# Kernel tuning notes

Measured on AMD Instinct MI355X. Metric: run time of the kernel, lower is better.

The kernel has to match this reference:

```python
import jax, jax.numpy as jnp
import numpy as np

RPN_NEG_OV = 0.3
RPN_POS_OV = 0.7
RPN_BATCHSIZE = 256
NUM_FG = int(0.5 * RPN_BATCHSIZE)  # RPN_FG_FRACTION * RPN_BATCHSIZE


def _generate_anchors(base_size=16, ratios=(0.5, 1, 2), scales=(8, 16, 32)):
    base = np.array([1, 1, base_size, base_size], dtype=np.float64) - 1
    w = base[2] - base[0] + 1
    h = base[3] - base[1] + 1
    x_ctr = base[0] + 0.5 * (w - 1)
    y_ctr = base[1] + 0.5 * (h - 1)
    anchors = []
    for r in ratios:
        wr = w * np.sqrt(r)
        hr = h / np.sqrt(r)
        for s in scales:
            sw, sh = wr * s, hr * s
            anchors.append([x_ctr - 0.5 * (sw - 1), y_ctr - 0.5 * (sh - 1),
                            x_ctr + 0.5 * (sw - 1), y_ctr + 0.5 * (sh - 1)])
    return np.array(anchors, dtype=np.float32)  # (9,4)


def setup_inputs() -> dict:
    key = jax.random.key(0)
    k1, k2, k3, k4, k5 = jax.random.split(key, 5)
    H = W = 160
    A = 9
    im_h = im_w = 2560.0
    M = 128
    # valid GT boxes: centers in image, sizes 64..512
    cx = jax.random.uniform(k1, (M,), minval=200.0, maxval=im_w - 200.0)
    cy = jax.random.uniform(k2, (M,), minval=200.0, maxval=im_h - 200.0)
    wh = jax.random.uniform(k3, (M, 2), minval=64.0, maxval=512.0)
    x1 = jnp.clip(cx - 0.5 * wh[:, 0], 0.0, im_w - 2)
    y1 = jnp.clip(cy - 0.5 * wh[:, 1], 0.0, im_h - 2)
    x2 = jnp.clip(cx + 0.5 * wh[:, 0], x1 + 1.0, im_w - 1)
    y2 = jnp.clip(cy + 0.5 * wh[:, 1], y1 + 1.0, im_h - 1)
    gt_boxes = jnp.stack([x1, y1, x2, y2, jnp.ones((M,))], axis=1).astype(jnp.float32)
    return {
        "rpn_cls_score": jax.random.normal(k4, (1, 2 * A, H, W), dtype=jnp.float32),
        "gt_boxes": gt_boxes,
        "im_info": jnp.array([[im_h, im_w, 1.0]], dtype=jnp.float32),
        "anchors": jnp.asarray(_generate_anchors()),
        "rand_fg": jax.random.uniform(k5, (H * W * A,), dtype=jnp.float32),
        "rand_bg": jax.random.uniform(jax.random.fold_in(k5, 1), (H * W * A,), dtype=jnp.float32),
        "feat_stride": 16,
    }


def _forward(rpn_cls_score, gt_boxes, im_info, anchors, rand_fg, rand_bg, feat_stride):
    H, W = rpn_cls_score.shape[-2:]
    A = anchors.shape[0]
    # --- all anchors on the grid: (K*A, 4) ---
    sx = (jnp.arange(W, dtype=jnp.float32) * feat_stride)
    sy = (jnp.arange(H, dtype=jnp.float32) * feat_stride)
    gy, gx = jnp.meshgrid(sy, sx, indexing="ij")
    shifts = jnp.stack([gx.ravel(), gy.ravel(), gx.ravel(), gy.ravel()], axis=1)  # (K,4)
    all_anchors = (anchors[None, :, :] + shifts[:, None, :]).reshape(-1, 4)  # (T,4)
    T = all_anchors.shape[0]
    im = im_info[0]
    inside = ((all_anchors[:, 0] >= 0) & (all_anchors[:, 1] >= 0)
              & (all_anchors[:, 2] < im[1]) & (all_anchors[:, 3] < im[0]))  # (T,)

    # --- pairwise IoU (T, M), +1 pixel convention as in bbox_overlaps ---
    ax1, ay1, ax2, ay2 = (all_anchors[:, i] for i in range(4))
    gx1, gy1, gx2, gy2 = (gt_boxes[:, i] for i in range(4))
    a_area = (ax2 - ax1 + 1.0) * (ay2 - ay1 + 1.0)           # (T,)
    g_area = (gx2 - gx1 + 1.0) * (gy2 - gy1 + 1.0)           # (M,)
    iw = jnp.minimum(ax2[:, None], gx2[None, :]) - jnp.maximum(ax1[:, None], gx1[None, :]) + 1.0
    ih = jnp.minimum(ay2[:, None], gy2[None, :]) - jnp.maximum(ay1[:, None], gy1[None, :]) + 1.0
    inter = jnp.maximum(iw, 0.0) * jnp.maximum(ih, 0.0)      # (T,M)
    ov = inter / (a_area[:, None] + g_area[None, :] - inter)
    # outside anchors never participate (original gathers inside anchors first)
    ov = jnp.where(inside[:, None], ov, -1.0)

    argmax_ov = jnp.argmax(ov, axis=1)                        # (T,)
    max_ov = jnp.max(ov, axis=1)                              # (T,)
    gt_max = jnp.max(ov, axis=0)                              # (M,)
    is_best = jnp.any(ov == gt_max[None, :], axis=1)          # anchors achieving per-gt max

    # --- label assignment (RPN_CLOBBER_POSITIVES=False) ---
    labels = jnp.full((T,), -1.0, dtype=jnp.float32)
    labels = jnp.where(inside & (max_ov < RPN_NEG_OV), 0.0, labels)
    labels = jnp.where(is_best, 1.0, labels)
    labels = jnp.where(inside & (max_ov >= RPN_POS_OV), 1.0, labels)

    # --- subsample fg via random priorities (== randperm semantics) ---
    fg = labels == 1.0
    pr = jnp.where(fg, rand_fg, 2.0)                           # non-fg sort last
    rank = jnp.argsort(jnp.argsort(pr))
    labels = jnp.where(fg & (rank >= NUM_FG), -1.0, labels)

    # --- subsample bg ---
    num_bg = RPN_BATCHSIZE - jnp.sum(labels == 1.0)
    bg = labels == 0.0
    pr2 = jnp.where(bg, rand_bg, 2.0)
    rank2 = jnp.argsort(jnp.argsort(pr2))
    labels = jnp.where(bg & (rank2 >= num_bg), -1.0, labels)

    g = gt_boxes[argmax_ov, :4]                                # (T,4)
    ew = ax2 - ax1 + 1.0
    eh = ay2 - ay1 + 1.0
    ecx = ax1 + 0.5 * ew
    ecy = ay1 + 0.5 * eh
    gw = g[:, 2] - g[:, 0] + 1.0
    gh = g[:, 3] - g[:, 1] + 1.0
    gcx = g[:, 0] + 0.5 * gw
    gcy = g[:, 1] + 0.5 * gh
    targets = jnp.stack([(gcx - ecx) / ew, (gcy - ecy) / eh,
                         jnp.log(gw / ew), jnp.log(gh / eh)], axis=1)
    targets = jnp.where(inside[:, None], targets, 0.0)

    # --- weights ---
    inside_w = jnp.where((labels == 1.0)[:, None], 1.0, 0.0)   # RPN_BBOX_INSIDE_WEIGHTS = 1s
    num_examples = jnp.sum(labels >= 0.0).astype(jnp.float32)
    wgt = jnp.where(num_examples > 0, 1.0 / jnp.maximum(num_examples, 1.0), 0.0)
    outside_w = jnp.where((labels >= 0.0)[:, None], wgt, 0.0)

    # pack: [label | bbox_targets(4) | inside_w(4) | outside_w(4)] -> (T,13)
    return jnp.concatenate([labels[:, None], targets, inside_w, outside_w], axis=1)


def reference(rpn_cls_score, gt_boxes, im_info, anchors, rand_fg, rand_bg, feat_stride):
    return _forward(rpn_cls_score, gt_boxes, im_info, anchors, rand_fg, rand_bg, feat_stride)
```

## Files before the change

### kernel.cpp

```cpp
#include <hip/hip_runtime.h>
#include <cstdint>


#define T_TOTAL 230400
#define W_ 160
#define A_ 9
#define M_ 128
#define NB_ 900
#define NBINS 4096
#define BCAP 1024
#define KFG 128
#define BATCH 256
#define SSTR 17

struct Ws {
  int gt_max_bits[M_];
  float4 g_box[M_];
  float g_area[M_];
  float amm[4];
  int fg_count, bg_count;
  int bnd_fg_n, bnd_bg_n;
  int sel_fg, b_fg, cb_fg;
  int sel_bg, b_bg, cb_bg, k_bg;
  float cut_fg_val; int cut_fg_idx;
  float cut_bg_val; int cut_bg_idx;
  float wgt;
  int hist_fg[NBINS], hist_bg[NBINS];
  float bnd_fg_val[BCAP]; int bnd_fg_idx[BCAP];
  float bnd_bg_val[BCAP]; int bnd_bg_idx[BCAP];
  unsigned char lab8[T_TOTAL];
  float t_soa[4][T_TOTAL];
  int blk_max[NB_ * M_];
  float best_v[T_TOTAL];
  int best_j[T_TOTAL];
};

__device__ __forceinline__ float fA(float a, float b) { return __fadd_rn(a, b); }
__device__ __forceinline__ float fS(float a, float b) { return __fsub_rn(a, b); }
__device__ __forceinline__ float fM(float a, float b) { return __fmul_rn(a, b); }
__device__ __forceinline__ float fD(float a, float b) { return __fdiv_rn(a, b); }

__device__ __forceinline__ int bucket_of(float v) {
  int b = (int)(v * 4096.0f);
  return b > (NBINS - 1) ? (NBINS - 1) : (b < 0 ? 0 : b);
}

__device__ __forceinline__ void anchor_coords(int i, const float* anch, float fs,
                                              float& ax1, float& ay1, float& ax2, float& ay2) {
  int s = i / A_, a = i - s * A_;
  int x = s % W_, y = s / W_;
  float shx = fM((float)x, fs), shy = fM((float)y, fs);
  ax1 = fA(anch[a * 4 + 0], shx);
  ay1 = fA(anch[a * 4 + 1], shy);
  ax2 = fA(anch[a * 4 + 2], shx);
  ay2 = fA(anch[a * 4 + 3], shy);
}

__device__ __forceinline__ void wave_bbox(int i0, const float* amm, float fs,
                                          float imw, float imh,
                                          float& wx1, float& wy1, float& wx2, float& wy2) {
  int s_lo = i0 / A_, s_hi = (i0 + 63) / A_;
  int y_lo = s_lo / W_, y_hi = s_hi / W_;
  int x_lo = s_lo - y_lo * W_, x_hi = s_hi - y_hi * W_;
  if (y_lo != y_hi) { x_lo = 0; x_hi = W_ - 1; }
  wx1 = fmaxf(amm[0] + fM((float)x_lo, fs), 0.0f);
  wy1 = fmaxf(amm[1] + fM((float)y_lo, fs), 0.0f);
  wx2 = fminf(amm[2] + fM((float)x_hi, fs), imw);
  wy2 = fminf(amm[3] + fM((float)y_hi, fs), imh);
}

__global__ __launch_bounds__(256) void k_init(const float* gt, const float* anch, Ws* ws) {
  int t = blockIdx.x * blockDim.x + threadIdx.x;
  int n = gridDim.x * blockDim.x;
  for (int i = t; i < NBINS; i += n) { ws->hist_fg[i] = 0; ws->hist_bg[i] = 0; }
  if (t < M_) {
    float x1 = gt[t * 5 + 0], y1 = gt[t * 5 + 1];
    float x2 = gt[t * 5 + 2], y2 = gt[t * 5 + 3];
    ws->g_box[t] = make_float4(x1, y1, x2, y2);
    ws->g_area[t] = fM(fA(fS(x2, x1), 1.0f), fA(fS(y2, y1), 1.0f));
  }
  if (t == 0) {
    float mx1 = anch[0], my1 = anch[1], Mx2 = anch[2], My2 = anch[3];
    for (int a = 1; a < A_; ++a) {
      mx1 = fminf(mx1, anch[a * 4 + 0]);
      my1 = fminf(my1, anch[a * 4 + 1]);
      Mx2 = fmaxf(Mx2, anch[a * 4 + 2]);
      My2 = fmaxf(My2, anch[a * 4 + 3]);
    }
    ws->amm[0] = mx1; ws->amm[1] = my1; ws->amm[2] = Mx2; ws->amm[3] = My2;
    ws->fg_count = 0; ws->bg_count = 0;
    ws->bnd_fg_n = 0; ws->bnd_bg_n = 0;
    ws->cut_fg_val = 2.0f; ws->cut_fg_idx = 0x7fffffff;
    ws->cut_bg_val = 2.0f; ws->cut_bg_idx = 0x7fffffff;
  }
}

__global__ __launch_bounds__(256) void k_sweep(
    const float4* __restrict__ gbox, const float* __restrict__ gap,
    const float* __restrict__ amm,
    const float* im_info, const float* anchors, const int* fsp,
    int* __restrict__ blk_max, float* __restrict__ best_v, int* __restrict__ best_j) {
  __shared__ int smax[M_ * SSTR];
  int tid = threadIdx.x;
  for (int s = tid; s < M_ * SSTR; s += 256) smax[s] = 0;
  __syncthreads();

  int lane = tid & 63, wv = tid >> 6;
  int slot = lane & 15;
  int i = blockIdx.x * 256 + tid;
  float fs = (float)fsp[0];
  float imh = im_info[0], imw = im_info[1];
  float ax1, ay1, ax2, ay2;
  anchor_coords(i, anchors, fs, ax1, ay1, ax2, ay2);
  bool inside = (ax1 >= 0.0f) && (ay1 >= 0.0f) && (ax2 < imw) && (ay2 < imh);
  float aarea;
  if (inside) {
    aarea = fM(fA(fS(ax2, ax1), 1.0f), fA(fS(ay2, ay1), 1.0f));
  } else {
    ax1 = 0.0f; ay1 = 0.0f; ax2 = -2.0f; ay2 = -2.0f; aarea = 1.0f;
  }

  float wx1, wy1, wx2, wy2;
  wave_bbox(blockIdx.x * 256 + wv * 64, amm, fs, imw, imh, wx1, wy1, wx2, wy2);
  float4 gA = gbox[lane];
  float4 gB = gbox[lane + 64];
  bool cA = (gA.x <= wx2 + 1.0f) && (gA.z + 1.0f >= wx1) &&
            (gA.y <= wy2 + 1.0f) && (gA.w + 1.0f >= wy1);
  bool cB = (gB.x <= wx2 + 1.0f) && (gB.z + 1.0f >= wx1) &&
            (gB.y <= wy2 + 1.0f) && (gB.w + 1.0f >= wy1);
  unsigned long long m0 = __ballot(cA);
  unsigned long long m1 = __ballot(cB);

  float bestv = 0.0f;
  int bestj = 0;
  auto body = [&](int j) {
    float4 g = gbox[j];
    float iw = fA(fS(fminf(ax2, g.z), fmaxf(ax1, g.x)), 1.0f);
    float ih = fA(fS(fminf(ay2, g.w), fmaxf(ay1, g.y)), 1.0f);
    float inter = fM(fmaxf(iw, 0.0f), fmaxf(ih, 0.0f));
    float uni = fS(fA(aarea, gap[j]), inter);
    float ov = fD(inter, uni);
    if (ov > bestv) { bestv = ov; bestj = j; }
    if (ov > 0.0f) atomicMax(&smax[j * SSTR + slot], __float_as_int(ov));
  };
  while (m0) { int j = __ffsll(m0) - 1; m0 &= (m0 - 1); body(j); }
  while (m1) { int j = __ffsll(m1) + 63; m1 &= (m1 - 1); body(j); }

  best_v[i] = bestv;
  best_j[i] = bestj;
  __syncthreads();
  if (tid < M_) {
    int m = 0;
#pragma unroll
    for (int s = 0; s < 16; ++s) {
      int v = smax[tid * SSTR + s];
      m = v > m ? v : m;
    }
    blk_max[blockIdx.x * M_ + tid] = m;
  }
}

__global__ __launch_bounds__(64) void k_reduce(const int* __restrict__ blk_max, int* gmb) {
  int j = blockIdx.x;
  int lane = threadIdx.x;
  int m = 0;
  for (int b = lane; b < NB_; b += 64) {
    int v = blk_max[b * M_ + j];
    m = v > m ? v : m;
  }
  m = max(m, __shfl_xor(m, 1));
  m = max(m, __shfl_xor(m, 2));
  m = max(m, __shfl_xor(m, 4));
  m = max(m, __shfl_xor(m, 8));
  m = max(m, __shfl_xor(m, 16));
  m = max(m, __shfl_xor(m, 32));
  if (lane == 0) gmb[j] = m;
}

__global__ __launch_bounds__(256) void k_labels(
    const float4* __restrict__ gbox, const float* __restrict__ gap,
    const float* __restrict__ amm, const int* __restrict__ gmb,
    const int* __restrict__ blk_max,
    const float* __restrict__ best_v, const int* __restrict__ best_j,
    const float* im_info, const float* anchors, const int* fsp,
    const float* rand_fg, const float* rand_bg,
    Ws* ws) {
  int tid = threadIdx.x;
  int lane = tid & 63, wv = tid >> 6;
  int i = blockIdx.x * 256 + tid;
  float fs = (float)fsp[0];
  float imh = im_info[0], imw = im_info[1];
  float rx1, ry1, rx2, ry2;
  anchor_coords(i, anchors, fs, rx1, ry1, rx2, ry2);
  bool inside = (rx1 >= 0.0f) && (ry1 >= 0.0f) && (rx2 < imw) && (ry2 < imh);
  float ax1 = rx1, ay1 = ry1, ax2 = rx2, ay2 = ry2, aarea;
  if (inside) {
    aarea = fM(fA(fS(ax2, ax1), 1.0f), fA(fS(ay2, ay1), 1.0f));
  } else {
    ax1 = 0.0f; ay1 = 0.0f; ax2 = -2.0f; ay2 = -2.0f; aarea = 1.0f;
  }

  float wx1, wy1, wx2, wy2;
  wave_bbox(blockIdx.x * 256 + wv * 64, amm, fs, imw, imh, wx1, wy1, wx2, wy2);
  float4 gA = gbox[lane];
  float4 gB = gbox[lane + 64];
  bool cA = (gA.x <= wx2 + 1.0f) && (gA.z + 1.0f >= wx1) &&
            (gA.y <= wy2 + 1.0f) && (gA.w + 1.0f >= wy1);
  bool cB = (gB.x <= wx2 + 1.0f) && (gB.z + 1.0f >= wx1) &&
            (gB.y <= wy2 + 1.0f) && (gB.w + 1.0f >= wy1);
  unsigned long long m0 = __ballot(cA);
  unsigned long long m1 = __ballot(cB);

  float bestv = best_v[i];
  int bestj = best_j[i];
  bool isbest = false;
  const int* bmrow = blk_max + blockIdx.x * M_;
  auto body = [&](int j) {
    int gm = gmb[j];
    if (bmrow[j] != gm) return;
    float4 g = gbox[j];
    float iw = fA(fS(fminf(ax2, g.z), fmaxf(ax1, g.x)), 1.0f);
    float ih = fA(fS(fminf(ay2, g.w), fmaxf(ay1, g.y)), 1.0f);
    float inter = fM(fmaxf(iw, 0.0f), fmaxf(ih, 0.0f));
    float uni = fS(fA(aarea, gap[j]), inter);
    float ov = fD(inter, uni);
    if (__float_as_int(ov) == gm) isbest = true;
  };
  while (m0) { int j = __ffsll(m0) - 1; m0 &= (m0 - 1); body(j); }
  while (m1) { int j = __ffsll(m1) + 63; m1 &= (m1 - 1); body(j); }
  isbest = isbest && inside;

  float lab = -1.0f;
  if (inside && bestv < 0.3f) lab = 0.0f;
  if (isbest) lab = 1.0f;
  if (inside && bestv >= 0.7f) lab = 1.0f;

  float t0 = 0.0f, t1 = 0.0f, t2 = 0.0f, t3 = 0.0f;
  if (inside) {
    float ew = fA(fS(rx2, rx1), 1.0f), eh = fA(fS(ry2, ry1), 1.0f);
    float ecx = fA(rx1, fM(0.5f, ew)), ecy = fA(ry1, fM(0.5f, eh));
    float4 g = gbox[bestj];
    float gw = fA(fS(g.z, g.x), 1.0f), gh = fA(fS(g.w, g.y), 1.0f);
    float gcx = fA(g.x, fM(0.5f, gw)), gcy = fA(g.y, fM(0.5f, gh));
    t0 = fD(fS(gcx, ecx), ew);
    t1 = fD(fS(gcy, ecy), eh);
    t2 = logf(fD(gw, ew));
    t3 = logf(fD(gh, eh));
  }

  ws->lab8[i] = lab == 1.0f ? 2 : (lab == 0.0f ? 1 : 0);
  ws->t_soa[0][i] = t0;
  ws->t_soa[1][i] = t1;
  ws->t_soa[2][i] = t2;
  ws->t_soa[3][i] = t3;

  if (lab == 1.0f) atomicAdd(&ws->hist_fg[bucket_of(rand_fg[i])], 1);
  if (lab == 0.0f) atomicAdd(&ws->hist_bg[bucket_of(rand_bg[i])], 1);
}

__global__ __launch_bounds__(256) void k_scan(Ws* ws) {
  __shared__ int part[256];
  __shared__ int s_fgc;
  int tid = threadIdx.x;
  for (int pass = 0; pass < 2; ++pass) {
    const int* hist = pass == 0 ? ws->hist_fg : ws->hist_bg;
    int sum = 0;
    for (int b = 0; b < NBINS / 256; ++b) sum += hist[tid * (NBINS / 256) + b];
    part[tid] = sum;
    __syncthreads();
    if (tid == 0) {
      int cnt = 0;
      for (int c = 0; c < 256; ++c) cnt += part[c];
      int k, kbg = 0;
      if (pass == 0) {
        s_fgc = cnt;
        ws->fg_count = cnt;
        k = KFG;
      } else {
        ws->bg_count = cnt;
        int kept_fg = s_fgc < KFG ? s_fgc : KFG;
        kbg = BATCH - kept_fg;
        k = kbg;
      }
      if (cnt > k) {
        int cum = 0, chunk = 0;
        for (int c = 0; c < 256; ++c) {
          if (cum + part[c] >= k + 1) { chunk = c; break; }
          cum += part[c];
        }
        int b = chunk * (NBINS / 256);
        for (int bb = chunk * (NBINS / 256); bb < (chunk + 1) * (NBINS / 256); ++bb) {
          if (cum + hist[bb] >= k + 1) { b = bb; break; }
          cum += hist[bb];
        }
        if (pass == 0) { ws->sel_fg = 1; ws->b_fg = b; ws->cb_fg = cum; }
        else           { ws->sel_bg = 1; ws->b_bg = b; ws->cb_bg = cum; }
      } else {
        if (pass == 0) { ws->sel_fg = 0; ws->b_fg = -1; ws->cb_fg = 0; }
        else           { ws->sel_bg = 0; ws->b_bg = -1; ws->cb_bg = 0; }
      }
      if (pass == 1) ws->k_bg = kbg;
    }
    __syncthreads();
  }
}

__global__ __launch_bounds__(256) void k_collect(const float* rand_fg, const float* rand_bg,
                                                 Ws* ws) {
  int i = blockIdx.x * 256 + threadIdx.x;
  int code = ws->lab8[i];
  if (code == 2 && ws->sel_fg) {
    float v = rand_fg[i];
    if (bucket_of(v) == ws->b_fg) {
      int p = atomicAdd(&ws->bnd_fg_n, 1);
      if (p < BCAP) { ws->bnd_fg_val[p] = v; ws->bnd_fg_idx[p] = i; }
    }
  }
  if (code == 1 && ws->sel_bg) {
    float v = rand_bg[i];
    if (bucket_of(v) == ws->b_bg) {
      int p = atomicAdd(&ws->bnd_bg_n, 1);
      if (p < BCAP) { ws->bnd_bg_val[p] = v; ws->bnd_bg_idx[p] = i; }
    }
  }
}

__global__ __launch_bounds__(256) void k_cut(Ws* ws) {
  __shared__ float sv[BCAP];
  __shared__ int si[BCAP];
  int tid = threadIdx.x;
  for (int pass = 0; pass < 2; ++pass) {
    int sel = pass == 0 ? ws->sel_fg : ws->sel_bg;
    if (sel) {
      int n_raw = pass == 0 ? ws->bnd_fg_n : ws->bnd_bg_n;
      int n = n_raw < BCAP ? n_raw : BCAP;
      int r = pass == 0 ? (KFG - ws->cb_fg) : (ws->k_bg - ws->cb_bg);
      const float* bv = pass == 0 ? ws->bnd_fg_val : ws->bnd_bg_val;
      const int* bi = pass == 0 ? ws->bnd_fg_idx : ws->bnd_bg_idx;
      for (int e = tid; e < n; e += 256) { sv[e] = bv[e]; si[e] = bi[e]; }
      __syncthreads();
      if (r >= 0 && r < n) {
        for (int e = tid; e < n; e += 256) {
          float ve = sv[e]; int ie = si[e];
          int c = 0;
          for (int o = 0; o < n; ++o) {
            float vo = sv[o]; int io = si[o];
            if (vo < ve || (vo == ve && io < ie)) c++;
          }
          if (c == r) {
            if (pass == 0) { ws->cut_fg_val = ve; ws->cut_fg_idx = ie; }
            else           { ws->cut_bg_val = ve; ws->cut_bg_idx = ie; }
          }
        }
      }
      __syncthreads();
    }
  }
  if (tid == 0) {
    int kept_fg = ws->sel_fg ? KFG : ws->fg_count;
    int kept_bg = ws->sel_bg ? ws->k_bg : ws->bg_count;
    int ne = kept_fg + kept_bg;
    ws->wgt = (ne > 0) ? __fdiv_rn(1.0f, (float)(ne < 1 ? 1 : ne)) : 0.0f;
  }
}

__global__ __launch_bounds__(256) void k_final(const float* rand_fg, const float* rand_bg,
                                               const Ws* __restrict__ ws, float* out) {
  __shared__ float sh[256][8];
  int tid = threadIdx.x;
  int i0 = blockIdx.x * 256;
  int i = i0 + tid;
  int code = ws->lab8[i];
  float lab = code == 2 ? 1.0f : (code == 1 ? 0.0f : -1.0f);
  if (code == 2 && ws->sel_fg) {
    float v = rand_fg[i];
    int b = bucket_of(v);
    float cv = ws->cut_fg_val; int ci = ws->cut_fg_idx;
    bool keep = (b < ws->b_fg) ||
                (b == ws->b_fg && (v < cv || (v == cv && i < ci)));
    if (!keep) lab = -1.0f;
  }
  if (code == 1 && ws->sel_bg) {
    float v = rand_bg[i];
    int b = bucket_of(v);
    float cv = ws->cut_bg_val; int ci = ws->cut_bg_idx;
    bool keep = (b < ws->b_bg) ||
                (b == ws->b_bg && (v < cv || (v == cv && i < ci)));
    if (!keep) lab = -1.0f;
  }
  sh[tid][0] = lab;
  sh[tid][1] = ws->t_soa[0][i];
  sh[tid][2] = ws->t_soa[1][i];
  sh[tid][3] = ws->t_soa[2][i];
  sh[tid][4] = ws->t_soa[3][i];
  sh[tid][5] = (lab == 1.0f) ? 1.0f : 0.0f;
  sh[tid][6] = (lab >= 0.0f) ? ws->wgt : 0.0f;
  __syncthreads();
#pragma unroll
  for (int k = 0; k < 7; ++k) {
    int l = k * 256 + tid;
    out[i0 * 7 + l] = sh[l / 7][l % 7];
  }
}

extern "C" void kernel_launch(void* const* d_in, const int* in_sizes, int n_in,
                              void* d_out, int out_size, void* d_ws, size_t ws_size,
                              hipStream_t stream) {
  const float* gt   = (const float*)d_in[1];
  const float* im   = (const float*)d_in[2];
  const float* anch = (const float*)d_in[3];
  const float* rfg  = (const float*)d_in[4];
  const float* rbg  = (const float*)d_in[5];
  const int*   fs   = (const int*)d_in[6];
  float* out = (float*)d_out;
  Ws* ws = (Ws*)d_ws;

  dim3 blk(256);
  int nb = NB_;
  k_init<<<17, blk, 0, stream>>>(gt, anch, ws);
  k_sweep<<<nb, blk, 0, stream>>>(ws->g_box, ws->g_area, ws->amm, im, anch, fs,
                                  ws->blk_max, ws->best_v, ws->best_j);
  k_reduce<<<M_, 64, 0, stream>>>(ws->blk_max, ws->gt_max_bits);
  k_labels<<<nb, blk, 0, stream>>>(ws->g_box, ws->g_area, ws->amm, ws->gt_max_bits,
                                   ws->blk_max, ws->best_v, ws->best_j,
                                   im, anch, fs, rfg, rbg, ws);
  k_scan<<<1, blk, 0, stream>>>(ws);
  k_collect<<<nb, blk, 0, stream>>>(rfg, rbg, ws);
  k_cut<<<1, blk, 0, stream>>>(ws);
  k_final<<<nb, blk, 0, stream>>>(rfg, rbg, ws, out);
}
```

Baseline: 57.77 us.

## Split IoU sweep across waves by GT subsets with 64-anchor blocks

Measured after the change: 62.87 us. +8.8%, slower.

```diff
diff --git a/kernel.cpp b/kernel.cpp
--- a/kernel.cpp
+++ b/kernel.cpp
@@ -7,6 +7,7 @@
 #define A_ 9
 #define M_ 128
 #define NB_ 900
+#define NSB_ 3600
 #define NBINS 4096
 #define BCAP 1024
 #define KFG 128
@@ -30,7 +31,7 @@
   float bnd_bg_val[BCAP]; int bnd_bg_idx[BCAP];
   unsigned char lab8[T_TOTAL];
   float t_soa[4][T_TOTAL];
-  int blk_max[NB_ * M_];
+  int blk_max[NSB_ * M_];
   float best_v[T_TOTAL];
   int best_j[T_TOTAL];
 };
@@ -101,13 +102,15 @@
     const float* im_info, const float* anchors, const int* fsp,
     int* __restrict__ blk_max, float* __restrict__ best_v, int* __restrict__ best_j) {
   __shared__ int smax[M_ * SSTR];
+  __shared__ float pv[4][64];
+  __shared__ int   pj[4][64];
   int tid = threadIdx.x;
   for (int s = tid; s < M_ * SSTR; s += 256) smax[s] = 0;
   __syncthreads();
 
   int lane = tid & 63, wv = tid >> 6;
   int slot = lane & 15;
-  int i = blockIdx.x * 256 + tid;
+  int i = blockIdx.x * 64 + lane;
   float fs = (float)fsp[0];
   float imh = im_info[0], imw = im_info[1];
   float ax1, ay1, ax2, ay2;
@@ -121,19 +124,19 @@
   }
 
   float wx1, wy1, wx2, wy2;
-  wave_bbox(blockIdx.x * 256 + wv * 64, amm, fs, imw, imh, wx1, wy1, wx2, wy2);
-  float4 gA = gbox[lane];
-  float4 gB = gbox[lane + 64];
-  bool cA = (gA.x <= wx2 + 1.0f) && (gA.z + 1.0f >= wx1) &&
-            (gA.y <= wy2 + 1.0f) && (gA.w + 1.0f >= wy1);
-  bool cB = (gB.x <= wx2 + 1.0f) && (gB.z + 1.0f >= wx1) &&
-            (gB.y <= wy2 + 1.0f) && (gB.w + 1.0f >= wy1);
-  unsigned long long m0 = __ballot(cA);
-  unsigned long long m1 = __ballot(cB);
+  wave_bbox(blockIdx.x * 64, amm, fs, imw, imh, wx1, wy1, wx2, wy2);
+  int jb = (wv << 5) + (lane & 31);
+  float4 gt_ = gbox[jb];
+  bool cand = (gt_.x <= wx2 + 1.0f) && (gt_.z + 1.0f >= wx1) &&
+              (gt_.y <= wy2 + 1.0f) && (gt_.w + 1.0f >= wy1);
+  unsigned mask = (unsigned)__ballot(cand);
 
   float bestv = 0.0f;
   int bestj = 0;
-  auto body = [&](int j) {
+  while (mask) {
+    int b = __ffs(mask) - 1;
+    mask &= mask - 1;
+    int j = (wv << 5) + b;
     float4 g = gbox[j];
     float iw = fA(fS(fminf(ax2, g.z), fmaxf(ax1, g.x)), 1.0f);
     float ih = fA(fS(fminf(ay2, g.w), fmaxf(ay1, g.y)), 1.0f);
@@ -142,13 +145,21 @@
     float ov = fD(inter, uni);
     if (ov > bestv) { bestv = ov; bestj = j; }
     if (ov > 0.0f) atomicMax(&smax[j * SSTR + slot], __float_as_int(ov));
-  };
-  while (m0) { int j = __ffsll(m0) - 1; m0 &= (m0 - 1); body(j); }
-  while (m1) { int j = __ffsll(m1) + 63; m1 &= (m1 - 1); body(j); }
-
-  best_v[i] = bestv;
-  best_j[i] = bestj;
+  }
+  pv[wv][lane] = bestv;
+  pj[wv][lane] = bestj;
   __syncthreads();
+
+  if (tid < 64) {
+    float rv = pv[0][tid]; int rj = pj[0][tid];
+#pragma unroll
+    for (int w = 1; w < 4; ++w) {
+      float v2 = pv[w][tid];
+      if (v2 > rv) { rv = v2; rj = pj[w][tid]; }
+    }
+    best_v[blockIdx.x * 64 + tid] = rv;
+    best_j[blockIdx.x * 64 + tid] = rj;
+  }
   if (tid < M_) {
     int m = 0;
 #pragma unroll
@@ -160,21 +171,22 @@
   }
 }
 
-__global__ __launch_bounds__(64) void k_reduce(const int* __restrict__ blk_max, int* gmb) {
+__global__ __launch_bounds__(256) void k_reduce(const int* __restrict__ blk_max, int* gmb) {
+  __shared__ int red[256];
   int j = blockIdx.x;
-  int lane = threadIdx.x;
+  int tid = threadIdx.x;
   int m = 0;
-  for (int b = lane; b < NB_; b += 64) {
+  for (int b = tid; b < NSB_; b += 256) {
     int v = blk_max[b * M_ + j];
     m = v > m ? v : m;
   }
-  m = max(m, __shfl_xor(m, 1));
-  m = max(m, __shfl_xor(m, 2));
-  m = max(m, __shfl_xor(m, 4));
-  m = max(m, __shfl_xor(m, 8));
-  m = max(m, __shfl_xor(m, 16));
-  m = max(m, __shfl_xor(m, 32));
-  if (lane == 0) gmb[j] = m;
+  red[tid] = m;
+  __syncthreads();
+  for (int s = 128; s > 0; s >>= 1) {
+    if (tid < s) { int v = red[tid + s]; if (v > red[tid]) red[tid] = v; }
+    __syncthreads();
+  }
+  if (tid == 0) gmb[j] = red[0];
 }
 
 __global__ __launch_bounds__(256) void k_labels(
@@ -214,7 +226,7 @@
   float bestv = best_v[i];
   int bestj = best_j[i];
   bool isbest = false;
-  const int* bmrow = blk_max + blockIdx.x * M_;
+  const int* bmrow = blk_max + (blockIdx.x * 4 + wv) * M_;
   auto body = [&](int j) {
     int gm = gmb[j];
     if (bmrow[j] != gm) return;
@@ -416,16 +428,15 @@
   Ws* ws = (Ws*)d_ws;
 
   dim3 blk(256);
-  int nb = NB_;
   k_init<<<17, blk, 0, stream>>>(gt, anch, ws);
-  k_sweep<<<nb, blk, 0, stream>>>(ws->g_box, ws->g_area, ws->amm, im, anch, fs,
-                                  ws->blk_max, ws->best_v, ws->best_j);
-  k_reduce<<<M_, 64, 0, stream>>>(ws->blk_max, ws->gt_max_bits);
-  k_labels<<<nb, blk, 0, stream>>>(ws->g_box, ws->g_area, ws->amm, ws->gt_max_bits,
-                                   ws->blk_max, ws->best_v, ws->best_j,
-                                   im, anch, fs, rfg, rbg, ws);
+  k_sweep<<<NSB_, blk, 0, stream>>>(ws->g_box, ws->g_area, ws->amm, im, anch, fs,
+                                    ws->blk_max, ws->best_v, ws->best_j);
+  k_reduce<<<M_, blk, 0, stream>>>(ws->blk_max, ws->gt_max_bits);
+  k_labels<<<NB_, blk, 0, stream>>>(ws->g_box, ws->g_area, ws->amm, ws->gt_max_bits,
+                                    ws->blk_max, ws->best_v, ws->best_j,
+                                    im, anch, fs, rfg, rbg, ws);
   k_scan<<<1, blk, 0, stream>>>(ws);
-  k_collect<<<nb, blk, 0, stream>>>(rfg, rbg, ws);
+  k_collect<<<NB_, blk, 0, stream>>>(rfg, rbg, ws);
   k_cut<<<1, blk, 0, stream>>>(ws);
-  k_final<<<nb, blk, 0, stream>>>(rfg, rbg, ws, out);
-}
+  k_final<<<NB_, blk, 0, stream>>>(rfg, rbg, ws, out);
+}
```

## Fuse provisional labeling into sweep and add sparse per-GT-best fixup kernel

Applied to the files above, without the earlier changes.

Measured after the change: 51.09 us (median of 2 runs). 1.13x faster.

```diff
diff --git a/kernel.cpp b/kernel.cpp
--- a/kernel.cpp
+++ b/kernel.cpp
@@ -31,8 +31,6 @@
   unsigned char lab8[T_TOTAL];
   float t_soa[4][T_TOTAL];
   int blk_max[NB_ * M_];
-  float best_v[T_TOTAL];
-  int best_j[T_TOTAL];
 };
 
 __device__ __forceinline__ float fA(float a, float b) { return __fadd_rn(a, b); }
@@ -99,7 +97,8 @@
     const float4* __restrict__ gbox, const float* __restrict__ gap,
     const float* __restrict__ amm,
     const float* im_info, const float* anchors, const int* fsp,
-    int* __restrict__ blk_max, float* __restrict__ best_v, int* __restrict__ best_j) {
+    const float* rand_fg, const float* rand_bg,
+    int* __restrict__ blk_max, Ws* ws) {
   __shared__ int smax[M_ * SSTR];
   int tid = threadIdx.x;
   for (int s = tid; s < M_ * SSTR; s += 256) smax[s] = 0;
@@ -110,10 +109,10 @@
   int i = blockIdx.x * 256 + tid;
   float fs = (float)fsp[0];
   float imh = im_info[0], imw = im_info[1];
-  float ax1, ay1, ax2, ay2;
-  anchor_coords(i, anchors, fs, ax1, ay1, ax2, ay2);
-  bool inside = (ax1 >= 0.0f) && (ay1 >= 0.0f) && (ax2 < imw) && (ay2 < imh);
-  float aarea;
+  float rx1, ry1, rx2, ry2;
+  anchor_coords(i, anchors, fs, rx1, ry1, rx2, ry2);
+  bool inside = (rx1 >= 0.0f) && (ry1 >= 0.0f) && (rx2 < imw) && (ry2 < imh);
+  float ax1 = rx1, ay1 = ry1, ax2 = rx2, ay2 = ry2, aarea;
   if (inside) {
     aarea = fM(fA(fS(ax2, ax1), 1.0f), fA(fS(ay2, ay1), 1.0f));
   } else {
@@ -146,93 +145,8 @@
   while (m0) { int j = __ffsll(m0) - 1; m0 &= (m0 - 1); body(j); }
   while (m1) { int j = __ffsll(m1) + 63; m1 &= (m1 - 1); body(j); }
 
-  best_v[i] = bestv;
-  best_j[i] = bestj;
-  __syncthreads();
-  if (tid < M_) {
-    int m = 0;
-#pragma unroll
-    for (int s = 0; s < 16; ++s) {
-      int v = smax[tid * SSTR + s];
-      m = v > m ? v : m;
-    }
-    blk_max[blockIdx.x * M_ + tid] = m;
-  }
-}
-
-__global__ __launch_bounds__(64) void k_reduce(const int* __restrict__ blk_max, int* gmb) {
-  int j = blockIdx.x;
-  int lane = threadIdx.x;
-  int m = 0;
-  for (int b = lane; b < NB_; b += 64) {
-    int v = blk_max[b * M_ + j];
-    m = v > m ? v : m;
-  }
-  m = max(m, __shfl_xor(m, 1));
-  m = max(m, __shfl_xor(m, 2));
-  m = max(m, __shfl_xor(m, 4));
-  m = max(m, __shfl_xor(m, 8));
-  m = max(m, __shfl_xor(m, 16));
-  m = max(m, __shfl_xor(m, 32));
-  if (lane == 0) gmb[j] = m;
-}
-
-__global__ __launch_bounds__(256) void k_labels(
-    const float4* __restrict__ gbox, const float* __restrict__ gap,
-    const float* __restrict__ amm, const int* __restrict__ gmb,
-    const int* __restrict__ blk_max,
-    const float* __restrict__ best_v, const int* __restrict__ best_j,
-    const float* im_info, const float* anchors, const int* fsp,
-    const float* rand_fg, const float* rand_bg,
-    Ws* ws) {
-  int tid = threadIdx.x;
-  int lane = tid & 63, wv = tid >> 6;
-  int i = blockIdx.x * 256 + tid;
-  float fs = (float)fsp[0];
-  float imh = im_info[0], imw = im_info[1];
-  float rx1, ry1, rx2, ry2;
-  anchor_coords(i, anchors, fs, rx1, ry1, rx2, ry2);
-  bool inside = (rx1 >= 0.0f) && (ry1 >= 0.0f) && (rx2 < imw) && (ry2 < imh);
-  float ax1 = rx1, ay1 = ry1, ax2 = rx2, ay2 = ry2, aarea;
-  if (inside) {
-    aarea = fM(fA(fS(ax2, ax1), 1.0f), fA(fS(ay2, ay1), 1.0f));
-  } else {
-    ax1 = 0.0f; ay1 = 0.0f; ax2 = -2.0f; ay2 = -2.0f; aarea = 1.0f;
-  }
-
-  float wx1, wy1, wx2, wy2;
-  wave_bbox(blockIdx.x * 256 + wv * 64, amm, fs, imw, imh, wx1, wy1, wx2, wy2);
-  float4 gA = gbox[lane];
-  float4 gB = gbox[lane + 64];
-  bool cA = (gA.x <= wx2 + 1.0f) && (gA.z + 1.0f >= wx1) &&
-            (gA.y <= wy2 + 1.0f) && (gA.w + 1.0f >= wy1);
-  bool cB = (gB.x <= wx2 + 1.0f) && (gB.z + 1.0f >= wx1) &&
-            (gB.y <= wy2 + 1.0f) && (gB.w + 1.0f >= wy1);
-  unsigned long long m0 = __ballot(cA);
-  unsigned long long m1 = __ballot(cB);
-
-  float bestv = best_v[i];
-  int bestj = best_j[i];
-  bool isbest = false;
-  const int* bmrow = blk_max + blockIdx.x * M_;
-  auto body = [&](int j) {
-    int gm = gmb[j];
-    if (bmrow[j] != gm) return;
-    float4 g = gbox[j];
-    float iw = fA(fS(fminf(ax2, g.z), fmaxf(ax1, g.x)), 1.0f);
-    float ih = fA(fS(fminf(ay2, g.w), fmaxf(ay1, g.y)), 1.0f);
-    float inter = fM(fmaxf(iw, 0.0f), fmaxf(ih, 0.0f));
-    float uni = fS(fA(aarea, gap[j]), inter);
-    float ov = fD(inter, uni);
-    if (__float_as_int(ov) == gm) isbest = true;
-  };
-  while (m0) { int j = __ffsll(m0) - 1; m0 &= (m0 - 1); body(j); }
-  while (m1) { int j = __ffsll(m1) + 63; m1 &= (m1 - 1); body(j); }
-  isbest = isbest && inside;
-
   float lab = -1.0f;
   if (inside && bestv < 0.3f) lab = 0.0f;
-  if (isbest) lab = 1.0f;
   if (inside && bestv >= 0.7f) lab = 1.0f;
 
   float t0 = 0.0f, t1 = 0.0f, t2 = 0.0f, t3 = 0.0f;
@@ -253,9 +167,88 @@
   ws->t_soa[1][i] = t1;
   ws->t_soa[2][i] = t2;
   ws->t_soa[3][i] = t3;
-
   if (lab == 1.0f) atomicAdd(&ws->hist_fg[bucket_of(rand_fg[i])], 1);
   if (lab == 0.0f) atomicAdd(&ws->hist_bg[bucket_of(rand_bg[i])], 1);
+
+  __syncthreads();
+  if (tid < M_) {
+    int m = 0;
+#pragma unroll
+    for (int s = 0; s < 16; ++s) {
+      int v = smax[tid * SSTR + s];
+      m = v > m ? v : m;
+    }
+    blk_max[blockIdx.x * M_ + tid] = m;
+  }
+}
+
+__global__ __launch_bounds__(64) void k_reduce(const int* __restrict__ blk_max, int* gmb) {
+  int j = blockIdx.x;
+  int lane = threadIdx.x;
+  int m = 0;
+  for (int b = lane; b < NB_; b += 64) {
+    int v = blk_max[b * M_ + j];
+    m = v > m ? v : m;
+  }
+  m = max(m, __shfl_xor(m, 1));
+  m = max(m, __shfl_xor(m, 2));
+  m = max(m, __shfl_xor(m, 4));
+  m = max(m, __shfl_xor(m, 8));
+  m = max(m, __shfl_xor(m, 16));
+  m = max(m, __shfl_xor(m, 32));
+  if (lane == 0) gmb[j] = m;
+}
+
+__global__ __launch_bounds__(256) void k_fixup(
+    const float4* __restrict__ gbox, const float* __restrict__ gap,
+    const int* __restrict__ gmb, const int* __restrict__ blk_max,
+    const float* im_info, const float* anchors, const int* fsp,
+    const float* rand_fg, const float* rand_bg, Ws* ws) {
+  __shared__ int fl[M_];
+  __shared__ int nfl;
+  int tid = threadIdx.x;
+  if (tid == 0) nfl = 0;
+  __syncthreads();
+  const int* bmrow = blk_max + blockIdx.x * M_;
+  if (tid < M_) {
+    int gm = gmb[tid];
+    if (gm > 0 && bmrow[tid] == gm) fl[atomicAdd(&nfl, 1)] = tid;
+  }
+  __syncthreads();
+  int n = nfl;
+  if (n == 0) return;
+
+  int i = blockIdx.x * 256 + tid;
+  float fs = (float)fsp[0];
+  float imh = im_info[0], imw = im_info[1];
+  float ax1, ay1, ax2, ay2;
+  anchor_coords(i, anchors, fs, ax1, ay1, ax2, ay2);
+  bool inside = (ax1 >= 0.0f) && (ay1 >= 0.0f) && (ax2 < imw) && (ay2 < imh);
+  float aarea;
+  if (inside) {
+    aarea = fM(fA(fS(ax2, ax1), 1.0f), fA(fS(ay2, ay1), 1.0f));
+  } else {
+    ax1 = 0.0f; ay1 = 0.0f; ax2 = -2.0f; ay2 = -2.0f; aarea = 1.0f;
+  }
+  bool isbest = false;
+  for (int k = 0; k < n; ++k) {
+    int j = fl[k];
+    float4 g = gbox[j];
+    float iw = fA(fS(fminf(ax2, g.z), fmaxf(ax1, g.x)), 1.0f);
+    float ih = fA(fS(fminf(ay2, g.w), fmaxf(ay1, g.y)), 1.0f);
+    float inter = fM(fmaxf(iw, 0.0f), fmaxf(ih, 0.0f));
+    float uni = fS(fA(aarea, gap[j]), inter);
+    float ov = fD(inter, uni);
+    if (__float_as_int(ov) == gmb[j]) isbest = true;
+  }
+  if (isbest && inside) {
+    int old = ws->lab8[i];
+    if (old != 2) {
+      ws->lab8[i] = 2;
+      atomicAdd(&ws->hist_fg[bucket_of(rand_fg[i])], 1);
+      if (old == 1) atomicSub(&ws->hist_bg[bucket_of(rand_bg[i])], 1);
+    }
+  }
 }
 
 __global__ __launch_bounds__(256) void k_scan(Ws* ws) {
@@ -416,16 +409,14 @@
   Ws* ws = (Ws*)d_ws;
 
   dim3 blk(256);
-  int nb = NB_;
   k_init<<<17, blk, 0, stream>>>(gt, anch, ws);
-  k_sweep<<<nb, blk, 0, stream>>>(ws->g_box, ws->g_area, ws->amm, im, anch, fs,
-                                  ws->blk_max, ws->best_v, ws->best_j);
+  k_sweep<<<NB_, blk, 0, stream>>>(ws->g_box, ws->g_area, ws->amm, im, anch, fs,
+                                   rfg, rbg, ws->blk_max, ws);
   k_reduce<<<M_, 64, 0, stream>>>(ws->blk_max, ws->gt_max_bits);
-  k_labels<<<nb, blk, 0, stream>>>(ws->g_box, ws->g_area, ws->amm, ws->gt_max_bits,
-                                   ws->blk_max, ws->best_v, ws->best_j,
+  k_fixup<<<NB_, blk, 0, stream>>>(ws->g_box, ws->g_area, ws->gt_max_bits, ws->blk_max,
                                    im, anch, fs, rfg, rbg, ws);
   k_scan<<<1, blk, 0, stream>>>(ws);
-  k_collect<<<nb, blk, 0, stream>>>(rfg, rbg, ws);
+  k_collect<<<NB_, blk, 0, stream>>>(rfg, rbg, ws);
   k_cut<<<1, blk, 0, stream>>>(ws);
-  k_final<<<nb, blk, 0, stream>>>(rfg, rbg, ws, out);
-}
+  k_final<<<NB_, blk, 0, stream>>>(rfg, rbg, ws, out);
+}
```
